# Performance work log

Measured on AMD Instinct MI355X. Metric: run time of the kernel, lower is better.

## Reference

```python
import jax, jax.numpy as jnp
from jax import lax
import numpy as np
import math

A = 9          # anchors per location
NC = 80        # classes
SCORE_T = 0.05
NMS_T = 0.5
DPI = 100      # detections_per_img (also per-level K in _inference)
BBOX_CLIP = math.log(1000.0 / 16.0)
LEVEL_SHAPES = [(64, 64), (32, 32), (16, 16), (8, 8)]
STRIDES = [8, 16, 32, 64]
BASE_SIZES = [32, 64, 128, 256]


def _conv(x, w, b):
    y = lax.conv_general_dilated(x, w, (1, 1), 'SAME', dimension_numbers=('NCHW', 'OIHW', 'NCHW'))
    return y + b[None, :, None, None]


def _head(feats, tower_w, tower_b, out_w, out_b, out_dim):
    outs = []
    for f in feats:
        x = f
        for i in range(tower_w.shape[0]):
            x = jax.nn.relu(_conv(x, tower_w[i], tower_b[i]))
        x = _conv(x, out_w, out_b)                     # [B, A*out_dim, H, W]
        B, _, H, W = x.shape
        x = x.reshape(B, A, out_dim, H, W).transpose(0, 3, 4, 1, 2).reshape(B, H * W * A, out_dim)
        outs.append(x)
    return outs


def _clip_boxes(b, img_h, img_w):
    x1 = jnp.clip(b[:, 0], 0.0, float(img_w)); y1 = jnp.clip(b[:, 1], 0.0, float(img_h))
    x2 = jnp.clip(b[:, 2], 0.0, float(img_w)); y2 = jnp.clip(b[:, 3], 0.0, float(img_h))
    return jnp.stack([x1, y1, x2, y2], axis=-1)


def _level_anchors(H, W, stride, s, img_h, img_w):
    # torchvision AnchorGenerator: sizes (s, s*2^(1/3), s*2^(2/3)), ratios (0.5,1,2)
    sizes = jnp.array([s, int(s * 2 ** (1 / 3)), int(s * 2 ** (2 / 3))], dtype=jnp.float32)
    ratios = jnp.array([0.5, 1.0, 2.0], dtype=jnp.float32)
    h_r = jnp.sqrt(ratios); w_r = 1.0 / h_r
    ws = (w_r[:, None] * sizes[None, :]).reshape(-1)
    hs = (h_r[:, None] * sizes[None, :]).reshape(-1)
    base = jnp.round(jnp.stack([-ws, -hs, ws, hs], axis=-1) / 2.0)   # [9,4]
    sx = (jnp.arange(W) * stride).astype(jnp.float32)
    sy = (jnp.arange(H) * stride).astype(jnp.float32)
    yy, xx = jnp.meshgrid(sy, sx, indexing='ij')
    shifts = jnp.stack([xx, yy, xx, yy], axis=-1).reshape(-1, 1, 4)   # [H*W,1,4]
    anch = (shifts + base[None]).reshape(-1, 4)                        # [H*W*A,4]
    return _clip_boxes(anch, img_h, img_w)


def _decode(rel, anch):
    # BoxCoder.decode_single with weights (1,1,1,1)
    w = anch[:, 2] - anch[:, 0]; h = anch[:, 3] - anch[:, 1]
    cx = anch[:, 0] + 0.5 * w;   cy = anch[:, 1] + 0.5 * h
    dx, dy = rel[:, 0], rel[:, 1]
    dw = jnp.minimum(rel[:, 2], BBOX_CLIP)
    dh = jnp.minimum(rel[:, 3], BBOX_CLIP)
    pcx = dx * w + cx; pcy = dy * h + cy
    pw = jnp.exp(dw) * w; ph = jnp.exp(dh) * h
    return jnp.stack([pcx - 0.5 * pw, pcy - 0.5 * ph, pcx + 0.5 * pw, pcy + 0.5 * ph], axis=-1)


def _pairwise_iou(boxes):
    area = (boxes[:, 2] - boxes[:, 0]) * (boxes[:, 3] - boxes[:, 1])
    lt = jnp.maximum(boxes[:, None, :2], boxes[None, :, :2])
    rb = jnp.minimum(boxes[:, None, 2:], boxes[None, :, 2:])
    wh = jnp.clip(rb - lt, 0.0)
    inter = wh[..., 0] * wh[..., 1]
    return inter / (area[:, None] + area[None, :] - inter + 1e-9)


def _per_image(logits, regs, anchors, img_h, img_w):
    bs, ss, ls = [], [], []
    for logit, reg, anch in zip(logits, regs, anchors):
        scores = jax.nn.sigmoid(logit).reshape(-1)                   # [N*NC]
        masked = jnp.where(scores > SCORE_T, scores, -1.0)
        top_s, idx = lax.top_k(masked, DPI)                          # fixed K = detections_per_img
        aidx = idx // NC
        lbl = idx % NC
        boxes = _clip_boxes(_decode(reg[aidx], anch[aidx]), img_h, img_w)
        valid = top_s > SCORE_T
        bs.append(boxes)
        ss.append(jnp.where(valid, top_s, -1.0))
        ls.append(jnp.where(valid, lbl, -1))
    boxes = jnp.concatenate(bs, 0); scores = jnp.concatenate(ss, 0); labels = jnp.concatenate(ls, 0)
    # batched (per-class) NMS via label coordinate offsets
    order = jnp.argsort(-scores)
    boxes_s = boxes[order]; scores_s = scores[order]; labels_s = labels[order]
    offset = labels_s.astype(boxes.dtype) * (float(max(img_h, img_w)) + 1.0)
    iou = lax.stop_gradient(_pairwise_iou(boxes_s + offset[:, None]))
    N = scores_s.shape[0]
    ar = jnp.arange(N)
    def body(i, keep):
        sup = keep[i] & (iou[i] > NMS_T) & (ar > i)
        return keep & ~sup
    keep = lax.fori_loop(0, N, body, scores_s > SCORE_T)
    fs, fi = lax.top_k(jnp.where(keep, scores_s, -1.0), DPI)
    ok = fs > SCORE_T
    fb = jnp.where(ok[:, None], boxes_s[fi], 0.0)
    fl = jnp.where(ok, labels_s[fi], -1)
    fs = jnp.where(ok, fs, 0.0)
    return fb, fs, fl


def setup_inputs() -> dict:
    key = jax.random.key(0)
    ks = jax.random.split(key, 8)
    B = 4
    w_scale = 0.04
    inp = {}
    shapes = [(B, 256, 64, 64), (B, 256, 32, 32), (B, 256, 16, 16), (B, 256, 8, 8)]
    for i, sh in enumerate(shapes):
        inp[f'f{i}'] = jax.random.normal(ks[i], sh, dtype=jnp.float32)
    inp['cls_tower_w'] = jax.random.normal(ks[4], (4, 256, 256, 3, 3), dtype=jnp.float32) * w_scale
    inp['cls_tower_b'] = jnp.zeros((4, 256), dtype=jnp.float32)
    inp['cls_out_w'] = jax.random.normal(ks[5], (A * NC, 256, 3, 3), dtype=jnp.float32) * w_scale
    inp['cls_out_b'] = jnp.full((A * NC,), -2.0, dtype=jnp.float32)  # prior-like bias
    inp['reg_tower_w'] = jax.random.normal(ks[6], (4, 256, 256, 3, 3), dtype=jnp.float32) * w_scale
    inp['reg_tower_b'] = jnp.zeros((4, 256), dtype=jnp.float32)
    inp['reg_out_w'] = jax.random.normal(ks[7], (A * 4, 256, 3, 3), dtype=jnp.float32) * w_scale
    inp['reg_out_b'] = jnp.zeros((A * 4,), dtype=jnp.float32)
    inp['image_h'] = 512
    inp['image_w'] = 512
    return inp


def reference(f0, f1, f2, f3, cls_tower_w, cls_tower_b, cls_out_w, cls_out_b,
              reg_tower_w, reg_tower_b, reg_out_w, reg_out_b, image_h, image_w):
    feats = [f0, f1, f2, f3]
    cls_logits = _head(feats, cls_tower_w, cls_tower_b, cls_out_w, cls_out_b, NC)   # list of [B,Ni,NC]
    bbox_regs = _head(feats, reg_tower_w, reg_tower_b, reg_out_w, reg_out_b, 4)     # list of [B,Ni,4]
    anchors = [_level_anchors(H, W, st, s, image_h, image_w)
               for (H, W), st, s in zip(LEVEL_SHAPES, STRIDES, BASE_SIZES)]
    fn = lambda ls, rs: _per_image(ls, rs, anchors, image_h, image_w)
    boxes, scores, labels = jax.vmap(fn)(tuple(cls_logits), tuple(bbox_regs))
    return boxes, scores, labels
```

## Files before the change

kernel.cpp:

```cpp
#include <hip/hip_runtime.h>
#include <math.h>

#define A_NUM 9
#define NCLS 80
#define IMG_KEY 3916800
#define IMG_REG 195840
#define CAP 8192
#define HBINS 16384

#define CHUNK_SLOTS 24064
#define CHUNK_BYTES (CHUNK_SLOTS * 16)
#define ACT_SLAB ((size_t)CHUNK_BYTES * 16)
#define WCHUNK_BYTES 40960
#define WCOG_BYTES (WCHUNK_BYTES * 16)

typedef _Float16 h8 __attribute__((ext_vector_type(8)));
typedef float fx4 __attribute__((ext_vector_type(4)));
typedef unsigned short u16;

__constant__ int   c_W[4]       = {64, 32, 16, 8};
__constant__ int   c_stride[4]  = {8, 16, 32, 64};
__constant__ float c_sizes[4][3]= {{32.f,40.f,50.f},{64.f,80.f,101.f},{128.f,161.f,203.f},{256.f,322.f,406.f}};
__constant__ int   c_keyOff[4]  = {0, 2949120, 3686400, 3870720};
__constant__ int   c_keyCnt[4]  = {2949120, 737280, 184320, 46080};
__constant__ int   c_regOff[4]  = {0, 147456, 184320, 193536};
__constant__ int   c_C[4]       = {66, 34, 18, 18};
__constant__ int   c_lvlSlot[4] = {0, 17424, 22048, 23344};
__constant__ int   c_pOff[4]    = {0, 1024, 1280, 1344};

__device__ __forceinline__ void gl_lds16(const void* g, void* l) {
    __builtin_amdgcn_global_load_lds(
        (const __attribute__((address_space(1))) void*)g,
        (__attribute__((address_space(3))) void*)l, 16, 0, 0);
}

__global__ __launch_bounds__(256) void pad16_k(
    const float* __restrict__ f0, const float* __restrict__ f1,
    const float* __restrict__ f2, const float* __restrict__ f3,
    char* __restrict__ Pin)
{
    int idx = blockIdx.x * 256 + threadIdx.x;
    const int PER_IMG = 16 * 2 * 1360;
    if (idx >= 4 * PER_IMG) return;
    int img = idx / PER_IMG;
    int r = idx - img * PER_IMG;
    int chunk = r / (2 * 1360);
    int r2 = r - chunk * (2 * 1360);
    int hfsel = r2 / 1360;
    int p = r2 - hfsel * 1360;
    int lvl = (p < 1024) ? 0 : (p < 1280 ? 1 : (p < 1344 ? 2 : 3));
    int u = p - c_pOff[lvl];
    int sh = 4 - lvl;
    int y = u >> sh;
    int xg = u & ((1 << sh) - 1);
    int x0 = xg * 4;
    int W = 64 >> lvl;
    const float* f = (lvl == 0) ? f0 : (lvl == 1) ? f1 : (lvl == 2) ? f2 : f3;
    int ci0 = chunk * 16 + hfsel * 8;
    float4 v[8];
    #pragma unroll
    for (int j = 0; j < 8; ++j)
        v[j] = *reinterpret_cast<const float4*>(
            f + ((size_t)(img * 256 + ci0 + j)) * (W * W) + y * W + x0);
    char* base = Pin + (size_t)img * ACT_SLAB + (size_t)chunk * CHUNK_BYTES;
    const int C = c_C[lvl];
    size_t rowSlot = (size_t)c_lvlSlot[lvl] + (size_t)((y + 1) * 4 + hfsel) * C;
    #pragma unroll
    for (int c = 0; c < 4; ++c) {
        h8 hv, lv;
        #pragma unroll
        for (int j = 0; j < 8; ++j) {
            float val = (c == 0) ? v[j].x : (c == 1) ? v[j].y : (c == 2) ? v[j].z : v[j].w;
            _Float16 hh = (_Float16)val;
            hv[j] = hh;
            lv[j] = (_Float16)(val - (float)hh);
        }
        size_t slot = rowSlot + (x0 + c + 1);
        *reinterpret_cast<h8*>(base + slot * 16) = hv;
        *reinterpret_cast<h8*>(base + (slot + 2 * (size_t)C) * 16) = lv;
    }
}

__global__ __launch_bounds__(256) void repack16_k(
    const float* __restrict__ src, u16* __restrict__ dst,
    int C_out, int nCg, int total)
{
    int idx = blockIdx.x * 256 + threadIdx.x;
    if (idx >= total) return;
    int per = nCg * 16 * 1280;
    int layer = idx / per;
    int r = idx - layer * per;
    int cg = r / (16 * 1280);
    int r2 = r - cg * (16 * 1280);
    int chunk = r2 / 1280;
    int s = r2 - chunk * 1280;
    int co = s & 63;
    int r3 = s >> 6;
    int hfsel = r3 & 1;
    int kk = r3 >> 1;
    int coG = cg * 64 + co;
    float v[8];
    if (kk < 9 && coG < C_out) {
        const float* sp = src + ((size_t)(layer * C_out + coG)) * 2304
                        + (size_t)(chunk * 16 + hfsel * 8) * 9 + kk;
        #pragma unroll
        for (int j = 0; j < 8; ++j) v[j] = sp[j * 9];
    } else {
        #pragma unroll
        for (int j = 0; j < 8; ++j) v[j] = 0.f;
    }
    h8 hv, lv;
    #pragma unroll
    for (int j = 0; j < 8; ++j) {
        _Float16 hh = (_Float16)v[j];
        hv[j] = hh;
        lv[j] = (_Float16)(v[j] - (float)hh);
    }
    size_t e = ((size_t)((layer * nCg + cg) * 16 + chunk)) * 20480
             + (size_t)(kk >> 1) * 4096 + (size_t)(kk & 1) * 2048
             + (size_t)hfsel * 512 + (size_t)co * 8;
    *reinterpret_cast<h8*>(dst + e) = hv;
    *reinterpret_cast<h8*>(dst + e + 1024) = lv;
}

__global__ __launch_bounds__(256, 2) void conv16(
    const char* __restrict__ Pin, const char* __restrict__ bufIn, char* __restrict__ bufOut,
    const u16* __restrict__ repA, const float* __restrict__ bA,
    const u16* __restrict__ repB, const float* __restrict__ bB,
    unsigned* __restrict__ keys, float* __restrict__ regb,
    int mode, int usePin)
{
    const int tid = threadIdx.x;
    const int lane = tid & 63;
    const int wv = tid >> 6;

    int img, head, coBase, C_out, epi, tile;
    if (mode == 0) {
        int hw = blockIdx.x;
        int logical = (hw & 7) * 88 + (hw >> 3);
        int z = logical / 88;
        int rem = logical - z * 88;
        tile = rem >> 2;
        coBase = (rem & 3) * 64;
        img = z & 3; head = z >> 2;
        C_out = 256; epi = 0;
    } else {
        int hw = blockIdx.x;
        int logical = (hw & 7) * 143 + (hw >> 3);
        img = logical / 286;
        int rem = logical - img * 286;
        tile = rem / 13;
        int yy = rem - tile * 13;
        if (yy < 12) { head = 0; coBase = yy * 64; C_out = 720; epi = 1; }
        else         { head = 1; coBase = 0;       C_out = 36;  epi = 2; }
    }
    const float* bsel = head ? bB : bA;
    const u16* wsel = head ? repB : repA;
    const char* wBase = (const char*)wsel + (size_t)(coBase >> 6) * WCOG_BYTES;

    int lvl, ty, tx;
    if (tile < 16)      { lvl = 0; ty = tile >> 2; tx = tile & 3; }
    else if (tile < 20) { int u = tile - 16; lvl = 1; ty = u >> 1; tx = u & 1; }
    else if (tile == 20){ lvl = 2; ty = 0; tx = 0; }
    else                { lvl = 3; ty = 0; tx = 0; }
    const int W = 64 >> lvl;
    const int C = c_C[lvl];
    const int tileY = ty * 16, tileX = tx * 16;

    const char* srcB = usePin ? Pin + (size_t)img * ACT_SLAB
                              : bufIn + (size_t)(head * 4 + img) * ACT_SLAB;

    __shared__ alignas(16) char sA[20736];
    __shared__ alignas(16) char sB[40960];

    const int laneCol = lane & 15;
    const int g = lane >> 4;
    const int halfS = g & 1;
    const int tapS = g >> 1;
    int laneA[5];
    #pragma unroll
    for (int k = 0; k < 5; ++k) {
        int kk = 2 * k + tapS; if (kk > 8) kk = 8;
        int ky = kk / 3;
        int kx = kk - ky * 3;
        laneA[k] = ky * 1152 + halfS * 288 + (laneCol + kx) * 16;
    }
    const int laneB = tapS * 4096 + halfS * 1024 + laneCol * 16;

    int aByte[6]; bool aOk[6];
    #pragma unroll
    for (int p = 0; p < 6; ++p) {
        int s = tid + 256 * p;
        aOk[p] = (s < 1296);
        int sc = aOk[p] ? s : 1295;
        int row = sc / 72;
        int q = sc - row * 72;
        int pl = q / 36;
        int q2 = q - pl * 36;
        int hf = q2 / 18;
        int col = q2 - hf * 18;
        aByte[p] = (c_lvlSlot[lvl] + ((tileY + row) * 4 + pl * 2 + hf) * C
                    + tileX + col) * 16;
    }

    fx4 acc[4][4];
    #pragma unroll
    for (int mt = 0; mt < 4; ++mt)
        #pragma unroll
        for (int nt = 0; nt < 4; ++nt)
            acc[mt][nt] = (fx4){0.f, 0.f, 0.f, 0.f};

    #pragma unroll 1
    for (int ck = 0; ck < 16; ++ck) {
        const char* srcCk = srcB + (size_t)ck * CHUNK_BYTES;
        #pragma unroll
        for (int p = 0; p < 6; ++p)
            if (aOk[p]) gl_lds16(srcCk + aByte[p], (char*)sA + (wv * 64 + 256 * p) * 16);
        const char* wCk = wBase + (size_t)ck * WCHUNK_BYTES;
        for (int j = wv; j < 40; j += 4)
            gl_lds16(wCk + j * 1024 + lane * 16, (char*)sB + j * 1024);
        __syncthreads();

        #pragma unroll
        for (int k = 0; k < 5; ++k) {
            const char* bk = sB + k * 8192;
            h8 Bh[4], Bl[4];
            #pragma unroll
            for (int nt = 0; nt < 4; ++nt) {
                Bh[nt] = *reinterpret_cast<const h8*>(bk + nt * 256 + laneB);
                Bl[nt] = *reinterpret_cast<const h8*>(bk + 2048 + nt * 256 + laneB);
            }
            #pragma unroll
            for (int mt = 0; mt < 4; ++mt) {
                const char* am = sA + (wv * 4 + mt) * 1152 + laneA[k];
                h8 Ah = *reinterpret_cast<const h8*>(am);
                h8 Al = *reinterpret_cast<const h8*>(am + 576);
                #pragma unroll
                for (int nt = 0; nt < 4; ++nt) {
                    acc[mt][nt] = __builtin_amdgcn_mfma_f32_16x16x32_f16(Ah, Bh[nt], acc[mt][nt], 0, 0, 0);
                    acc[mt][nt] = __builtin_amdgcn_mfma_f32_16x16x32_f16(Ah, Bl[nt], acc[mt][nt], 0, 0, 0);
                    acc[mt][nt] = __builtin_amdgcn_mfma_f32_16x16x32_f16(Al, Bh[nt], acc[mt][nt], 0, 0, 0);
                }
            }
        }
        __syncthreads();
    }

    const int HW = W * W;
    if (epi == 0) {
        char* dstB = bufOut + (size_t)(head * 4 + img) * ACT_SLAB;
        _Float16* eW = reinterpret_cast<_Float16*>(sB + wv * 1024);
        const int ci8 = laneCol & 7;
        const int hf  = laneCol >> 3;
        const int rpx = lane & 15, rhalf = (lane >> 4) & 1, rplane = lane >> 5;
        const int rOff = rpx * 32 + rplane * 16 + rhalf * 8;
        const int rx = tileX + rpx;
        #pragma unroll
        for (int mt = 0; mt < 4; ++mt) {
            int y = tileY + wv * 4 + mt;
            bool yok = (y < W);
            #pragma unroll
            for (int nt = 0; nt < 4; ++nt) {
                int coG = coBase + nt * 16 + laneCol;
                float b = bsel[coG];
                #pragma unroll
                for (int i = 0; i < 4; ++i) {
                    float v = fmaxf(acc[mt][nt][i] + b, 0.f);
                    _Float16 hh = (_Float16)v;
                    _Float16 ll = (_Float16)(v - (float)hh);
                    int px = g * 4 + i;
                    eW[px * 32 + hf * 8 + ci8] = hh;
                    eW[px * 32 + 16 + hf * 8 + ci8] = ll;
                }
                __syncthreads();
                if (yok && rx < W) {
                    int chunkIdx = (coBase + nt * 16) >> 4;
                    size_t slot = (size_t)chunkIdx * CHUNK_SLOTS + c_lvlSlot[lvl]
                                + (size_t)(((y + 1) * 2 + rplane) * 2 + rhalf) * C + (rx + 1);
                    *reinterpret_cast<h8*>(dstB + slot * 16) =
                        *reinterpret_cast<const h8*>(eW + rOff);
                }
                __syncthreads();
            }
        }
    } else if (epi == 1) {
        unsigned* kb = keys + (size_t)img * IMG_KEY + c_keyOff[lvl];
        #pragma unroll
        for (int mt = 0; mt < 4; ++mt) {
            int y = tileY + wv * 4 + mt;
            int x0 = tileX + g * 4;
            if (y >= W || x0 >= W) continue;
            #pragma unroll
            for (int nt = 0; nt < 4; ++nt) {
                int coG = coBase + nt * 16 + laneCol;
                if (coG >= C_out) continue;
                float b = bsel[coG];
                unsigned kq[4];
                #pragma unroll
                for (int i = 0; i < 4; ++i) {
                    float sc = 1.0f / (1.0f + expf(-(acc[mt][nt][i] + b)));
                    kq[i] = (sc > 0.05f) ? __float_as_uint(sc) : 0u;
                }
                *reinterpret_cast<uint4*>(kb + (size_t)coG * HW + y * W + x0) =
                    make_uint4(kq[0], kq[1], kq[2], kq[3]);
            }
        }
    } else {
        float* rb = regb + (size_t)img * IMG_REG + c_regOff[lvl];
        #pragma unroll
        for (int mt = 0; mt < 4; ++mt) {
            int y = tileY + wv * 4 + mt;
            if (y >= W) continue;
            #pragma unroll
            for (int nt = 0; nt < 4; ++nt) {
                int coG = nt * 16 + laneCol;
                if (coG >= C_out) continue;
                float b = bsel[coG];
                int a = coG >> 2, jj = coG & 3;
                #pragma unroll
                for (int i = 0; i < 4; ++i) {
                    int x = tileX + g * 4 + i;
                    if (x >= W) continue;
                    rb[((size_t)(y * W + x) * A_NUM + a) * 4 + jj] = acc[mt][nt][i] + b;
                }
            }
        }
    }
}

__global__ __launch_bounds__(256) void hist_k(const unsigned* __restrict__ keys,
                                              unsigned* __restrict__ hist)
{
    int il = blockIdx.y, img = il >> 2, lvl = il & 3;
    int n = c_keyCnt[lvl];
    int chunk = blockIdx.x * 16384;
    if (chunk >= n) return;
    __shared__ unsigned h[HBINS];
    for (int t = threadIdx.x; t < HBINS; t += 256) h[t] = 0;
    __syncthreads();
    const uint4* k4 = (const uint4*)(keys + (size_t)img * IMG_KEY + c_keyOff[lvl]);
    int i0 = chunk >> 2, i1 = min(chunk + 16384, n) >> 2;
    for (int i = i0 + (int)threadIdx.x; i < i1; i += 256) {
        uint4 kv = k4[i];
        if (kv.x) atomicAdd(&h[kv.x >> 18], 1u);
        if (kv.y) atomicAdd(&h[kv.y >> 18], 1u);
        if (kv.z) atomicAdd(&h[kv.z >> 18], 1u);
        if (kv.w) atomicAdd(&h[kv.w >> 18], 1u);
    }
    __syncthreads();
    unsigned* gh = hist + (size_t)il * HBINS;
    for (int t = threadIdx.x; t < HBINS; t += 256)
        if (h[t]) atomicAdd(&gh[t], h[t]);
}

__global__ __launch_bounds__(256) void thresh_k(const unsigned* __restrict__ hist,
                                                unsigned* __restrict__ tbin)
{
    const unsigned* h = hist + (size_t)blockIdx.x * HBINS;
    __shared__ unsigned cs[256];
    int tid = threadIdx.x;
    unsigned s = 0;
    int base = tid * 64;
    for (int q = 0; q < 64; ++q) { int b = base + q; if (b >= 1) s += h[b]; }
    cs[tid] = s;
    __syncthreads();
    if (tid == 0) {
        unsigned total = 0, sel = 0;
        for (int c = 255; c >= 0; --c) {
            if (total + cs[c] >= 100u) {
                int lo = (c == 0) ? 1 : c * 64;
                for (int b = c * 64 + 63; b >= lo; --b) {
                    total += h[b];
                    if (total >= 100u) { sel = (unsigned)b; break; }
                }
                break;
            }
            total += cs[c];
        }
        tbin[blockIdx.x] = sel;
    }
}

__global__ __launch_bounds__(256) void compact_k(const unsigned* __restrict__ keys,
                                                 const unsigned* __restrict__ tbin,
                                                 unsigned* __restrict__ cnt,
                                                 uint2* __restrict__ comp)
{
    int il = blockIdx.y, img = il >> 2, lvl = il & 3;
    int n = c_keyCnt[lvl];
    int chunk = blockIdx.x * 16384;
    if (chunk >= n) return;
    const uint4* k4 = (const uint4*)(keys + (size_t)img * IMG_KEY + c_keyOff[lvl]);
    unsigned thr = tbin[il] << 18;
    int shift = 12 - 2 * lvl;
    int hwm = (1 << shift) - 1;
    int i0 = chunk >> 2, i1 = min(chunk + 16384, n) >> 2;
    __shared__ unsigned lcnt, lbase, lcur;
    if (threadIdx.x == 0) { lcnt = 0; lcur = 0; }
    __syncthreads();
    unsigned myc = 0;
    for (int i = i0 + (int)threadIdx.x; i < i1; i += 256) {
        uint4 kv = k4[i];
        myc += (kv.x != 0u && kv.x >= thr);
        myc += (kv.y != 0u && kv.y >= thr);
        myc += (kv.z != 0u && kv.z >= thr);
        myc += (kv.w != 0u && kv.w >= thr);
    }
    if (myc) atomicAdd(&lcnt, myc);
    __syncthreads();
    if (threadIdx.x == 0 && lcnt) lbase = atomicAdd(&cnt[il], lcnt);
    __syncthreads();
    if (lcnt == 0) return;
    uint2* c = comp + (size_t)il * CAP;
    for (int i = i0 + (int)threadIdx.x; i < i1; i += 256) {
        uint4 kv = k4[i];
        unsigned kk[4] = {kv.x, kv.y, kv.z, kv.w};
        #pragma unroll
        for (int j = 0; j < 4; ++j) {
            unsigned key = kk[j];
            if (key != 0u && key >= thr) {
                int t = i * 4 + j;
                int co = t >> shift, p = t & hwm;
                int a = co / NCLS, cls = co - a * NCLS;
                unsigned idx = (unsigned)((p * A_NUM + a) * NCLS + cls);
                unsigned pos = lbase + atomicAdd(&lcur, 1u);
                if (pos < CAP) c[pos] = make_uint2(key, idx);
            }
        }
    }
}

__global__ __launch_bounds__(256) void topsort_k(const unsigned* __restrict__ cnt,
                                                 const uint2* __restrict__ comp,
                                                 uint2* __restrict__ topk)
{
    __shared__ unsigned long long s[CAP];
    int il = blockIdx.x, tid = threadIdx.x;
    int n = (int)min(cnt[il], (unsigned)CAP);
    const uint2* c = comp + (size_t)il * CAP;
    for (int i = tid; i < CAP; i += 256) {
        unsigned long long v = 0ull;
        if (i < n) {
            uint2 e = c[i];
            v = ((unsigned long long)e.x << 32) | (unsigned long long)(~e.y);
        }
        s[i] = v;
    }
    for (int k = 2; k <= CAP; k <<= 1) {
        for (int j = k >> 1; j > 0; j >>= 1) {
            __syncthreads();
            for (int p = tid; p < CAP / 2; p += 256) {
                int i = ((p & ~(j - 1)) << 1) | (p & (j - 1));
                int ixj = i | j;
                unsigned long long a = s[i], b = s[ixj];
                if (((i & k) == 0) ? (a < b) : (a > b)) { s[i] = b; s[ixj] = a; }
            }
        }
    }
    __syncthreads();
    if (tid < 100) {
        unsigned long long v = s[tid];
        topk[il * 100 + tid] = make_uint2((unsigned)(v >> 32), ~(unsigned)(v & 0xFFFFFFFFull));
    }
}

__global__ void decode_k(const uint2* __restrict__ topk, const float* __restrict__ regb,
                         float* __restrict__ cboxes, float* __restrict__ cscores,
                         int* __restrict__ clabels, const int* __restrict__ ph, const int* __restrict__ pw)
{
    int il = blockIdx.x, img = il >> 2, lvl = il & 3;
    int j = threadIdx.x;
    if (j >= 100) return;
    float imgW = (float)pw[0], imgH = (float)ph[0];
    uint2 tk = topk[il * 100 + j];
    int outP = img * 400 + lvl * 100 + j;
    if (tk.x == 0u) {
        cboxes[outP * 4 + 0] = 0.f; cboxes[outP * 4 + 1] = 0.f;
        cboxes[outP * 4 + 2] = 0.f; cboxes[outP * 4 + 3] = 0.f;
        cscores[outP] = -1.0f; clabels[outP] = -1;
        return;
    }
    float score = __uint_as_float(tk.x);
    unsigned idx = tk.y;
    int aidx = (int)(idx / NCLS);
    int lbl  = (int)(idx - (unsigned)aidx * NCLS);
    int a = aidx % A_NUM, p = aidx / A_NUM;
    int W = c_W[lvl];
    int y = p / W, x = p - y * W;
    int r = a / 3, si = a - r * 3;
    float ratio = (r == 0) ? 0.5f : ((r == 1) ? 1.0f : 2.0f);
    float size = c_sizes[lvl][si];
    float hr = sqrtf(ratio);
    float wr = 1.0f / hr;
    float wsz = wr * size, hsz = hr * size;
    float bw = rintf(wsz * 0.5f), bh = rintf(hsz * 0.5f);
    float sx = (float)(x * c_stride[lvl]), sy = (float)(y * c_stride[lvl]);
    float ax1 = fminf(fmaxf(sx - bw, 0.f), imgW);
    float ay1 = fminf(fmaxf(sy - bh, 0.f), imgH);
    float ax2 = fminf(fmaxf(sx + bw, 0.f), imgW);
    float ay2 = fminf(fmaxf(sy + bh, 0.f), imgH);
    float aw = ax2 - ax1, ah = ay2 - ay1;
    float cx = ax1 + 0.5f * aw, cy = ay1 + 0.5f * ah;
    const float* rel = regb + (size_t)img * IMG_REG + c_regOff[lvl] + (size_t)aidx * 4;
    float dx = rel[0], dy = rel[1];
    float dw = fminf(rel[2], 4.135166556742356f);
    float dh = fminf(rel[3], 4.135166556742356f);
    float pcx = dx * aw + cx, pcy = dy * ah + cy;
    float pwd = expf(dw) * aw, phd = expf(dh) * ah;
    float x1 = pcx - 0.5f * pwd, y1 = pcy - 0.5f * phd;
    float x2 = pcx + 0.5f * pwd, y2 = pcy + 0.5f * phd;
    cboxes[outP * 4 + 0] = fminf(fmaxf(x1, 0.f), imgW);
    cboxes[outP * 4 + 1] = fminf(fmaxf(y1, 0.f), imgH);
    cboxes[outP * 4 + 2] = fminf(fmaxf(x2, 0.f), imgW);
    cboxes[outP * 4 + 3] = fminf(fmaxf(y2, 0.f), imgH);
    cscores[outP] = score;
    clabels[outP] = lbl;
}

__global__ __launch_bounds__(512) void nms_k(const float* __restrict__ cboxes,
                                             const float* __restrict__ cscores,
                                             const int* __restrict__ clabels,
                                             const int* __restrict__ ph, const int* __restrict__ pw,
                                             float* __restrict__ out)
{
    int img = blockIdx.x, tid = threadIdx.x;
    __shared__ float sSc[512];
    __shared__ int   sPos[512];
    __shared__ float bx1[400], by1[400], bx2[400], by2[400], sAr[400];
    __shared__ int   sKeep[400], sLbl[400];
    float imgH = (float)ph[0], imgW = (float)pw[0];
    float offm = fmaxf(imgH, imgW) + 1.0f;

    sSc[tid] = (tid < 400) ? cscores[img * 400 + tid] : -3.0f;
    sPos[tid] = tid;
    __syncthreads();

    for (int k = 2; k <= 512; k <<= 1) {
        for (int jj = k >> 1; jj > 0; jj >>= 1) {
            int ixj = tid ^ jj;
            if (ixj > tid) {
                float s1 = sSc[tid], s2 = sSc[ixj];
                int p1 = sPos[tid], p2 = sPos[ixj];
                bool bef = (s1 > s2) || (s1 == s2 && p1 < p2);
                bool sw = ((tid & k) == 0) ? (!bef) : bef;
                if (sw) { sSc[tid] = s2; sSc[ixj] = s1; sPos[tid] = p2; sPos[ixj] = p1; }
            }
            __syncthreads();
        }
    }

    if (tid < 400) {
        int p = sPos[tid];
        int lbl = clabels[img * 400 + p];
        float ofs = (float)lbl * offm;
        float x1 = cboxes[(img * 400 + p) * 4 + 0] + ofs;
        float y1 = cboxes[(img * 400 + p) * 4 + 1] + ofs;
        float x2 = cboxes[(img * 400 + p) * 4 + 2] + ofs;
        float y2 = cboxes[(img * 400 + p) * 4 + 3] + ofs;
        bx1[tid] = x1; by1[tid] = y1; bx2[tid] = x2; by2[tid] = y2;
        sAr[tid] = (x2 - x1) * (y2 - y1);
        sLbl[tid] = lbl;
        sKeep[tid] = (sSc[tid] > 0.05f) ? 1 : 0;
    }
    __syncthreads();

    for (int i = 0; i < 400; ++i) {
        if (sKeep[i]) {
            for (int j2 = i + 1 + tid; j2 < 400; j2 += 512) {
                float ltx = fmaxf(bx1[i], bx1[j2]), lty = fmaxf(by1[i], by1[j2]);
                float rbx = fminf(bx2[i], bx2[j2]), rby = fminf(by2[i], by2[j2]);
                float ww = fmaxf(rbx - ltx, 0.f), hh = fmaxf(rby - lty, 0.f);
                float inter = ww * hh;
                float iou = inter / (((sAr[i] + sAr[j2]) - inter) + 1e-9f);
                if (iou > 0.5f) sKeep[j2] = 0;
            }
        }
        __syncthreads();
    }

    if (tid == 0) {
        int rank = 0;
        for (int i = 0; i < 400 && rank < 100; ++i) {
            if (sKeep[i]) {
                int p = sPos[i];
                for (int kk = 0; kk < 4; ++kk)
                    out[(img * 100 + rank) * 4 + kk] = cboxes[(img * 400 + p) * 4 + kk];
                out[1600 + img * 100 + rank] = sSc[i];
                out[2000 + img * 100 + rank] = (float)sLbl[i];
                ++rank;
            }
        }
        for (; rank < 100; ++rank) {
            for (int kk = 0; kk < 4; ++kk) out[(img * 100 + rank) * 4 + kk] = 0.f;
            out[1600 + img * 100 + rank] = 0.f;
            out[2000 + img * 100 + rank] = -1.0f;
        }
    }
}

extern "C" void kernel_launch(void* const* d_in, const int* in_sizes, int n_in,
                              void* d_out, int out_size, void* d_ws, size_t ws_size,
                              hipStream_t stream)
{
    const float* f0 = (const float*)d_in[0];
    const float* f1 = (const float*)d_in[1];
    const float* f2 = (const float*)d_in[2];
    const float* f3 = (const float*)d_in[3];
    const float* cls_tw = (const float*)d_in[4];
    const float* cls_tb = (const float*)d_in[5];
    const float* cls_ow = (const float*)d_in[6];
    const float* cls_ob = (const float*)d_in[7];
    const float* reg_tw = (const float*)d_in[8];
    const float* reg_tb = (const float*)d_in[9];
    const float* reg_ow = (const float*)d_in[10];
    const float* reg_ob = (const float*)d_in[11];
    const int* ph = (const int*)d_in[12];
    const int* pw = (const int*)d_in[13];
    float* out = (float*)d_out;

    char* ws = (char*)d_ws;
    size_t off = 0;
    auto alloc = [&](size_t bytes) -> void* {
        void* p = ws + off;
        off = (off + bytes + 1023) & ~(size_t)1023;
        return p;
    };
    const size_t KEYS = (size_t)4 * IMG_KEY * 4;
    const size_t ACT8 = ACT_SLAB * 8;
    char*     Pin    = (char*)alloc(ACT_SLAB * 4 + 32768);
    char*     slabA  = (char*)alloc((KEYS > ACT8 ? KEYS : ACT8) + 32768);
    unsigned* keys   = (unsigned*)slabA;
    char*     actA   = slabA;
    char*     actB   = (char*)alloc(ACT8 + 32768);
    u16*      repCT  = (u16*)alloc((size_t)16 * WCOG_BYTES);
    u16*      repRT  = (u16*)alloc((size_t)16 * WCOG_BYTES);
    u16*      repCO  = (u16*)alloc((size_t)12 * WCOG_BYTES);
    u16*      repRO  = (u16*)alloc((size_t)1 * WCOG_BYTES);
    float*    regb   = (float*)alloc((size_t)4 * IMG_REG * 4);
    unsigned* hist   = (unsigned*)alloc((size_t)16 * HBINS * 4);
    unsigned* cnt    = (unsigned*)alloc(16 * 4);
    unsigned* tbin   = (unsigned*)alloc(16 * 4);
    uint2*    comp   = (uint2*)alloc((size_t)16 * CAP * 8);
    uint2*    topk   = (uint2*)alloc((size_t)1600 * 8);
    float*    cboxes = (float*)alloc((size_t)4 * 400 * 4 * 4);
    float*    cscores= (float*)alloc((size_t)4 * 400 * 4);
    int*      clabels= (int*)alloc((size_t)4 * 400 * 4);

    hipMemsetAsync(Pin, 0, ACT_SLAB * 4, stream);
    hipMemsetAsync(actA, 0, ACT8, stream);
    hipMemsetAsync(actB, 0, ACT8, stream);
    hipMemsetAsync(hist, 0, (size_t)16 * HBINS * 4, stream);
    hipMemsetAsync(cnt, 0, 64, stream);

    {
        int tPad = 4 * 16 * 2 * 1360;
        pad16_k<<<(tPad + 255) / 256, 256, 0, stream>>>(f0, f1, f2, f3, Pin);
        int tT = 4 * 4 * 16 * 1280;
        repack16_k<<<(tT + 255) / 256, 256, 0, stream>>>(cls_tw, repCT, 256, 4, tT);
        repack16_k<<<(tT + 255) / 256, 256, 0, stream>>>(reg_tw, repRT, 256, 4, tT);
        int tCO = 12 * 16 * 1280;
        repack16_k<<<(tCO + 255) / 256, 256, 0, stream>>>(cls_ow, repCO, 720, 12, tCO);
        int tRO = 16 * 1280;
        repack16_k<<<(tRO + 255) / 256, 256, 0, stream>>>(reg_ow, repRO, 36, 1, tRO);
    }

    const size_t RL = (size_t)4 * 16 * 20480;
    conv16<<<704, 256, 0, stream>>>(Pin, Pin, actA,
        repCT, cls_tb, repRT, reg_tb, keys, regb, 0, 1);
    conv16<<<704, 256, 0, stream>>>(Pin, actA, actB,
        repCT + RL, cls_tb + 256, repRT + RL, reg_tb + 256, keys, regb, 0, 0);
    conv16<<<704, 256, 0, stream>>>(Pin, actB, actA,
        repCT + 2 * RL, cls_tb + 512, repRT + 2 * RL, reg_tb + 512, keys, regb, 0, 0);
    conv16<<<704, 256, 0, stream>>>(Pin, actA, actB,
        repCT + 3 * RL, cls_tb + 768, repRT + 3 * RL, reg_tb + 768, keys, regb, 0, 0);
    conv16<<<1144, 256, 0, stream>>>(Pin, actB, nullptr,
        repCO, cls_ob, repRO, reg_ob, keys, regb, 1, 0);

    hist_k<<<dim3(180, 16), 256, 0, stream>>>(keys, hist);
    thresh_k<<<16, 256, 0, stream>>>(hist, tbin);
    compact_k<<<dim3(180, 16), 256, 0, stream>>>(keys, tbin, cnt, comp);
    topsort_k<<<16, 256, 0, stream>>>(cnt, comp, topk);
    decode_k<<<16, 128, 0, stream>>>(topk, regb, cboxes, cscores, clabels, ph, pw);
    nms_k<<<4, 512, 0, stream>>>(cboxes, cscores, clabels, ph, pw, out);
}
```

Before: 1.322 ms.

## Split hi/lo fp16 planes and read low parts directly from global to halve LDS

Reorganises the activation and weight layouts so the high and low fp16 halves live in separate planes. Only the high halves are staged in LDS. The low-half activations and weights are loaded straight from global memory into registers, with the weight low parts double-buffered across taps. Halving LDS use allows three blocks per CU instead of two, in exchange for more uncoalesced global and cache traffic and higher register pressure.

```diff
diff --git a/kernel.cpp b/kernel.cpp
--- a/kernel.cpp
+++ b/kernel.cpp
@@ -8,6 +8,7 @@
 #define CAP 8192
 #define HBINS 16384
 
+#define PCHUNK 12032
 #define CHUNK_SLOTS 24064
 #define CHUNK_BYTES (CHUNK_SLOTS * 16)
 #define ACT_SLAB ((size_t)CHUNK_BYTES * 16)
@@ -25,7 +26,7 @@
 __constant__ int   c_keyCnt[4]  = {2949120, 737280, 184320, 46080};
 __constant__ int   c_regOff[4]  = {0, 147456, 184320, 193536};
 __constant__ int   c_C[4]       = {66, 34, 18, 18};
-__constant__ int   c_lvlSlot[4] = {0, 17424, 22048, 23344};
+__constant__ int   c_plvl[4]    = {0, 8712, 11024, 11672};
 __constant__ int   c_pOff[4]    = {0, 1024, 1280, 1344};
 
 __device__ __forceinline__ void gl_lds16(const void* g, void* l) {
@@ -64,7 +65,7 @@
             f + ((size_t)(img * 256 + ci0 + j)) * (W * W) + y * W + x0);
     char* base = Pin + (size_t)img * ACT_SLAB + (size_t)chunk * CHUNK_BYTES;
     const int C = c_C[lvl];
-    size_t rowSlot = (size_t)c_lvlSlot[lvl] + (size_t)((y + 1) * 4 + hfsel) * C;
+    size_t rowSlot = (size_t)c_plvl[lvl] + (size_t)((y + 1) * 2 + hfsel) * C;
     #pragma unroll
     for (int c = 0; c < 4; ++c) {
         h8 hv, lv;
@@ -77,7 +78,7 @@
         }
         size_t slot = rowSlot + (x0 + c + 1);
         *reinterpret_cast<h8*>(base + slot * 16) = hv;
-        *reinterpret_cast<h8*>(base + (slot + 2 * (size_t)C) * 16) = lv;
+        *reinterpret_cast<h8*>(base + (slot + PCHUNK) * 16) = lv;
     }
 }
 
@@ -117,13 +118,13 @@
         lv[j] = (_Float16)(v[j] - (float)hh);
     }
     size_t e = ((size_t)((layer * nCg + cg) * 16 + chunk)) * 20480
-             + (size_t)(kk >> 1) * 4096 + (size_t)(kk & 1) * 2048
+             + (size_t)(kk >> 1) * 2048 + (size_t)(kk & 1) * 1024
              + (size_t)hfsel * 512 + (size_t)co * 8;
     *reinterpret_cast<h8*>(dst + e) = hv;
-    *reinterpret_cast<h8*>(dst + e + 1024) = lv;
-}
-
-__global__ __launch_bounds__(256, 2) void conv16(
+    *reinterpret_cast<h8*>(dst + e + 10240) = lv;
+}
+
+__global__ __launch_bounds__(256, 3) void conv16(
     const char* __restrict__ Pin, const char* __restrict__ bufIn, char* __restrict__ bufOut,
     const u16* __restrict__ repA, const float* __restrict__ bA,
     const u16* __restrict__ repB, const float* __restrict__ bB,
@@ -165,42 +166,45 @@
     else                { lvl = 3; ty = 0; tx = 0; }
     const int W = 64 >> lvl;
     const int C = c_C[lvl];
+    const int plvl = c_plvl[lvl];
     const int tileY = ty * 16, tileX = tx * 16;
 
     const char* srcB = usePin ? Pin + (size_t)img * ACT_SLAB
                               : bufIn + (size_t)(head * 4 + img) * ACT_SLAB;
 
-    __shared__ alignas(16) char sA[20736];
-    __shared__ alignas(16) char sB[40960];
+    __shared__ alignas(16) char sA[10368];
+    __shared__ alignas(16) char sB[20480];
 
     const int laneCol = lane & 15;
     const int g = lane >> 4;
     const int halfS = g & 1;
     const int tapS = g >> 1;
-    int laneA[5];
+    const int laneBv = tapS * 2048 + halfS * 1024 + laneCol * 16;
+    int laneAhi[5];
+    int AloOff[5];
     #pragma unroll
     for (int k = 0; k < 5; ++k) {
         int kk = 2 * k + tapS; if (kk > 8) kk = 8;
         int ky = kk / 3;
         int kx = kk - ky * 3;
-        laneA[k] = ky * 1152 + halfS * 288 + (laneCol + kx) * 16;
-    }
-    const int laneB = tapS * 4096 + halfS * 1024 + laneCol * 16;
-
-    int aByte[6]; bool aOk[6];
+        laneAhi[k] = ky * 576 + halfS * 288 + (laneCol + kx) * 16;
+        AloOff[k] = PCHUNK * 16
+                  + (plvl + ((tileY + wv * 4 + ky) * 2 + halfS) * C
+                     + tileX + laneCol + kx) * 16;
+    }
+    const int mtStride = 2 * C * 16;
+
+    int aByte[3]; bool aOk[3];
     #pragma unroll
-    for (int p = 0; p < 6; ++p) {
+    for (int p = 0; p < 3; ++p) {
         int s = tid + 256 * p;
-        aOk[p] = (s < 1296);
-        int sc = aOk[p] ? s : 1295;
-        int row = sc / 72;
-        int q = sc - row * 72;
-        int pl = q / 36;
-        int q2 = q - pl * 36;
-        int hf = q2 / 18;
-        int col = q2 - hf * 18;
-        aByte[p] = (c_lvlSlot[lvl] + ((tileY + row) * 4 + pl * 2 + hf) * C
-                    + tileX + col) * 16;
+        aOk[p] = (s < 648);
+        int sc = aOk[p] ? s : 647;
+        int row = sc / 36;
+        int q = sc - row * 36;
+        int hf = q / 18;
+        int col = q - hf * 18;
+        aByte[p] = (plvl + ((tileY + row) * 2 + hf) * C + tileX + col) * 16;
     }
 
     fx4 acc[4][4];
@@ -213,33 +217,46 @@
     #pragma unroll 1
     for (int ck = 0; ck < 16; ++ck) {
         const char* srcCk = srcB + (size_t)ck * CHUNK_BYTES;
-        #pragma unroll
-        for (int p = 0; p < 6; ++p)
+        const char* wCk = wBase + (size_t)ck * WCHUNK_BYTES;
+        const char* wLo = wCk + 20480;
+
+        h8 Bl[2][4];
+        #pragma unroll
+        for (int nt = 0; nt < 4; ++nt)
+            Bl[0][nt] = *reinterpret_cast<const h8*>(wLo + laneBv + nt * 256);
+
+        #pragma unroll
+        for (int p = 0; p < 3; ++p)
             if (aOk[p]) gl_lds16(srcCk + aByte[p], (char*)sA + (wv * 64 + 256 * p) * 16);
-        const char* wCk = wBase + (size_t)ck * WCHUNK_BYTES;
-        for (int j = wv; j < 40; j += 4)
+        for (int j = wv; j < 20; j += 4)
             gl_lds16(wCk + j * 1024 + lane * 16, (char*)sB + j * 1024);
         __syncthreads();
 
         #pragma unroll
         for (int k = 0; k < 5; ++k) {
-            const char* bk = sB + k * 8192;
-            h8 Bh[4], Bl[4];
+            if (k < 4) {
+                const char* wn = wLo + (k + 1) * 4096;
+                #pragma unroll
+                for (int nt = 0; nt < 4; ++nt)
+                    Bl[(k + 1) & 1][nt] = *reinterpret_cast<const h8*>(wn + laneBv + nt * 256);
+            }
+            h8 Al[4];
             #pragma unroll
-            for (int nt = 0; nt < 4; ++nt) {
-                Bh[nt] = *reinterpret_cast<const h8*>(bk + nt * 256 + laneB);
-                Bl[nt] = *reinterpret_cast<const h8*>(bk + 2048 + nt * 256 + laneB);
-            }
+            for (int mt = 0; mt < 4; ++mt)
+                Al[mt] = *reinterpret_cast<const h8*>(srcCk + AloOff[k] + mt * mtStride);
+            const char* bk = sB + k * 4096;
+            h8 Bh[4];
+            #pragma unroll
+            for (int nt = 0; nt < 4; ++nt)
+                Bh[nt] = *reinterpret_cast<const h8*>(bk + laneBv + nt * 256);
             #pragma unroll
             for (int mt = 0; mt < 4; ++mt) {
-                const char* am = sA + (wv * 4 + mt) * 1152 + laneA[k];
-                h8 Ah = *reinterpret_cast<const h8*>(am);
-                h8 Al = *reinterpret_cast<const h8*>(am + 576);
+                h8 Ah = *reinterpret_cast<const h8*>(sA + (wv * 4 + mt) * 576 + laneAhi[k]);
                 #pragma unroll
                 for (int nt = 0; nt < 4; ++nt) {
                     acc[mt][nt] = __builtin_amdgcn_mfma_f32_16x16x32_f16(Ah, Bh[nt], acc[mt][nt], 0, 0, 0);
-                    acc[mt][nt] = __builtin_amdgcn_mfma_f32_16x16x32_f16(Ah, Bl[nt], acc[mt][nt], 0, 0, 0);
-                    acc[mt][nt] = __builtin_amdgcn_mfma_f32_16x16x32_f16(Al, Bh[nt], acc[mt][nt], 0, 0, 0);
+                    acc[mt][nt] = __builtin_amdgcn_mfma_f32_16x16x32_f16(Ah, Bl[k & 1][nt], acc[mt][nt], 0, 0, 0);
+                    acc[mt][nt] = __builtin_amdgcn_mfma_f32_16x16x32_f16(Al[mt], Bh[nt], acc[mt][nt], 0, 0, 0);
                 }
             }
         }
@@ -275,8 +292,8 @@
                 __syncthreads();
                 if (yok && rx < W) {
                     int chunkIdx = (coBase + nt * 16) >> 4;
-                    size_t slot = (size_t)chunkIdx * CHUNK_SLOTS + c_lvlSlot[lvl]
-                                + (size_t)(((y + 1) * 2 + rplane) * 2 + rhalf) * C + (rx + 1);
+                    size_t slot = (size_t)chunkIdx * CHUNK_SLOTS + (size_t)rplane * PCHUNK
+                                + plvl + (size_t)((y + 1) * 2 + rhalf) * C + (rx + 1);
                     *reinterpret_cast<h8*>(dstB + slot * 16) =
                         *reinterpret_cast<const h8*>(eW + rOff);
                 }
```

Measured after the change: 1.316 ms, median of 2. No clear change (-0.4%).
